# Kernel tuning notes

Measured on AMD Instinct MI355X. Metric: run time of the kernel, lower is better.

Reference implementation:

```python
import jax, jax.numpy as jnp
import numpy as np

NOISE_STD = 0.5
NOISE_VAR = NOISE_STD ** 2  # softmax temperature = 1 / noise_variance

N, C, H, W = 256, 3, 32, 32
M = 50000


def setup_inputs() -> dict:
    key = jax.random.key(0)
    k1, k2 = jax.random.split(key)
    x = jax.random.normal(k1, (N, C, H, W), dtype=jnp.float32)
    dataset = jax.random.normal(k2, (M, C, H, W), dtype=jnp.float32)
    return {"x": x, "dataset": dataset}


def reference(x, dataset):
    # Flatten: x -> [N, D], dataset -> [M, D]
    n = x.shape[0]
    input_shape = dataset.shape[1:]
    xf = x.reshape(n, -1)
    df = dataset.reshape(dataset.shape[0], -1)
    # scores = x . dataset^T / noise_variance, softmax over dataset axis
    scores = jnp.einsum("nd,md->nm", xf, df) / NOISE_VAR  # [N, M]
    w = jax.nn.softmax(scores, axis=-1)
    # Weighted average of dataset points: [N, D]
    out = jnp.einsum("nm,md->nd", w, df)
    return out.reshape((n,) + input_shape)
```

## Files before the change

### kernel.cpp

```cpp
#include <hip/hip_runtime.h>
#include <stdint.h>
#include <stddef.h>

#define N_Q 256
#define M_D 50000
#define K_D 3072
#define MTILE 64
#define BK 32
#define CAND_CAP 128
#define WINDOW 9.0f

typedef short bf16x8 __attribute__((ext_vector_type(8)));
typedef float f32x4 __attribute__((ext_vector_type(4)));

static __device__ inline unsigned short f2bf(float f) {
    unsigned int u = __float_as_uint(f);
    u += 0x7fffu + ((u >> 16) & 1u);
    return (unsigned short)(u >> 16);
}

__global__ __launch_bounds__(256) void cvt_x_kernel(const float* __restrict__ x,
                                                    short* __restrict__ xb) {
    int i = (blockIdx.x * 256 + threadIdx.x) * 4;
    float4 f = *(const float4*)(x + i);
    ushort4 o;
    o.x = f2bf(f.x); o.y = f2bf(f.y); o.z = f2bf(f.z); o.w = f2bf(f.w);
    *(ushort4*)(xb + i) = o;
}

__global__ __launch_bounds__(256) void gemm_scores(const short* __restrict__ xb,
                                                   const float* __restrict__ dset,
                                                   float* __restrict__ scores) {
    __shared__ __align__(16) short sA[N_Q * BK];
    __shared__ __align__(16) short sB[MTILE * BK];

    const int tid = threadIdx.x;
    const int w = tid >> 6;
    const int l = tid & 63;
    const int m0 = blockIdx.x * MTILE;

    f32x4 acc[4][4];
#pragma unroll
    for (int i = 0; i < 4; ++i)
#pragma unroll
        for (int j = 0; j < 4; ++j)
            acc[i][j] = (f32x4){0.f, 0.f, 0.f, 0.f};

    const int br = tid >> 2;
    const int bq = tid & 3;
    const bool bvalid = (m0 + br) < M_D;
    const float* bsrc = dset + (size_t)(m0 + br) * K_D + bq * 8;

    const int kk = (l >> 4) * 8;
    const int rA = l & 15;

    for (int kt = 0; kt < K_D / BK; ++kt) {
        __syncthreads();

#pragma unroll
        for (int j = 0; j < 4; ++j) {
            int c = j * 256 + tid;
            int row = c >> 2;
            int off = c & 3;
            bf16x8 v = *(const bf16x8*)(xb + (size_t)row * K_D + kt * BK + off * 8);
            *(bf16x8*)&sA[c * 8] = v;
        }
        {
            bf16x8 pk;
            if (bvalid) {
                const float* p = bsrc + kt * BK;
                float4 f0 = *(const float4*)p;
                float4 f1 = *(const float4*)(p + 4);
                pk[0] = (short)f2bf(f0.x); pk[1] = (short)f2bf(f0.y);
                pk[2] = (short)f2bf(f0.z); pk[3] = (short)f2bf(f0.w);
                pk[4] = (short)f2bf(f1.x); pk[5] = (short)f2bf(f1.y);
                pk[6] = (short)f2bf(f1.z); pk[7] = (short)f2bf(f1.w);
            } else {
                pk = (bf16x8){0, 0, 0, 0, 0, 0, 0, 0};
            }
            *(bf16x8*)&sB[br * BK + bq * 8] = pk;
        }
        __syncthreads();

        bf16x8 af[4], bfr[4];
#pragma unroll
        for (int ai = 0; ai < 4; ++ai)
            af[ai] = *(const bf16x8*)&sA[(w * 64 + ai * 16 + rA) * BK + kk];
#pragma unroll
        for (int bj = 0; bj < 4; ++bj)
            bfr[bj] = *(const bf16x8*)&sB[(bj * 16 + rA) * BK + kk];
#pragma unroll
        for (int ai = 0; ai < 4; ++ai)
#pragma unroll
            for (int bj = 0; bj < 4; ++bj)
                acc[ai][bj] = __builtin_amdgcn_mfma_f32_16x16x32_bf16(
                    af[ai], bfr[bj], acc[ai][bj], 0, 0, 0);
    }

    const int crow = (l >> 4) * 4;
    const int ccol = l & 15;
#pragma unroll
    for (int ai = 0; ai < 4; ++ai) {
#pragma unroll
        for (int bj = 0; bj < 4; ++bj) {
            int m = m0 + bj * 16 + ccol;
            if (m < M_D) {
#pragma unroll
                for (int r = 0; r < 4; ++r) {
                    int n = w * 64 + ai * 16 + crow + r;
                    scores[(size_t)n * M_D + m] = acc[ai][bj][r];
                }
            }
        }
    }
}

__global__ __launch_bounds__(256) void scan_rows(const float* __restrict__ scores,
                                                 int* __restrict__ cidx,
                                                 int* __restrict__ ccnt) {
    const int n = blockIdx.x;
    const int tid = threadIdx.x;
    const float4* row4 = (const float4*)(scores + (size_t)n * M_D);

    float mx = -3.0e38f;
    for (int m4 = tid; m4 < M_D / 4; m4 += 256) {
        float4 v = row4[m4];
        mx = fmaxf(mx, fmaxf(fmaxf(v.x, v.y), fmaxf(v.z, v.w)));
    }
#pragma unroll
    for (int off = 32; off > 0; off >>= 1) mx = fmaxf(mx, __shfl_down(mx, off));

    __shared__ float wred[4];
    __shared__ int cnt;
    if ((tid & 63) == 0) wred[tid >> 6] = mx;
    if (tid == 0) cnt = 0;
    __syncthreads();
    float rowmax = fmaxf(fmaxf(wred[0], wred[1]), fmaxf(wred[2], wred[3]));
    float thr = rowmax - WINDOW;

    for (int m4 = tid; m4 < M_D / 4; m4 += 256) {
        float4 v = row4[m4];
        if (v.x >= thr || v.y >= thr || v.z >= thr || v.w >= thr) {
            float e[4] = {v.x, v.y, v.z, v.w};
#pragma unroll
            for (int j = 0; j < 4; ++j) {
                if (e[j] >= thr) {
                    int p = atomicAdd(&cnt, 1);
                    if (p < CAND_CAP) cidx[n * CAND_CAP + p] = m4 * 4 + j;
                }
            }
        }
    }
    __syncthreads();
    if (tid == 0) ccnt[n] = cnt < CAND_CAP ? cnt : CAND_CAP;
}

__global__ __launch_bounds__(256) void finalize_rows(const float* __restrict__ x,
                                                     const float* __restrict__ dset,
                                                     const int* __restrict__ cidx,
                                                     const int* __restrict__ ccnt,
                                                     float* __restrict__ out) {
    const int n = blockIdx.x;
    const int tid = threadIdx.x;
    const int cnt = ccnt[n];

    __shared__ float L[CAND_CAP];
    __shared__ float wred[4];
    const float4* xr4 = (const float4*)(x + (size_t)n * K_D);

    for (int c = 0; c < cnt; ++c) {
        const float4* dr4 = (const float4*)(dset + (size_t)cidx[n * CAND_CAP + c] * K_D);
        float p = 0.f;
        for (int j = tid; j < K_D / 4; j += 256) {
            float4 a = xr4[j], b = dr4[j];
            p += a.x * b.x + a.y * b.y + a.z * b.z + a.w * b.w;
        }
#pragma unroll
        for (int off = 32; off > 0; off >>= 1) p += __shfl_down(p, off);
        if ((tid & 63) == 0) wred[tid >> 6] = p;
        __syncthreads();
        if (tid == 0) L[c] = 4.0f * (wred[0] + wred[1] + wred[2] + wred[3]);
        __syncthreads();
    }

    if (tid == 0) {
        float mx = -3.0e38f;
        for (int c = 0; c < cnt; ++c) mx = fmaxf(mx, L[c]);
        float s = 0.f;
        for (int c = 0; c < cnt; ++c) { float e = expf(L[c] - mx); L[c] = e; s += e; }
        float inv = 1.0f / s;
        for (int c = 0; c < cnt; ++c) L[c] *= inv;
    }
    __syncthreads();

    float4* out4 = (float4*)(out + (size_t)n * K_D);
    for (int j = tid; j < K_D / 4; j += 256) {
        float4 o = {0.f, 0.f, 0.f, 0.f};
        for (int c = 0; c < cnt; ++c) {
            float wc = L[c];
            float4 d = *(const float4*)(dset + (size_t)cidx[n * CAND_CAP + c] * K_D + j * 4);
            o.x += wc * d.x; o.y += wc * d.y; o.z += wc * d.z; o.w += wc * d.w;
        }
        out4[j] = o;
    }
}

extern "C" void kernel_launch(void* const* d_in, const int* in_sizes, int n_in,
                              void* d_out, int out_size, void* d_ws, size_t ws_size,
                              hipStream_t stream) {
    const float* x = (const float*)d_in[0];
    const float* dset = (const float*)d_in[1];
    float* out = (float*)d_out;

    char* ws = (char*)d_ws;
    short* xb = (short*)ws;
    float* scores = (float*)(ws + 1572864);
    int* cidx = (int*)(ws + 1572864 + 51200000);
    int* ccnt = (int*)(ws + 1572864 + 51200000 + 131072);

    cvt_x_kernel<<<768, 256, 0, stream>>>(x, xb);
    gemm_scores<<<(M_D + MTILE - 1) / MTILE, 256, 0, stream>>>(xb, dset, scores);
    scan_rows<<<N_Q, 256, 0, stream>>>(scores, cidx, ccnt);
    finalize_rows<<<N_Q, 256, 0, stream>>>(x, dset, cidx, ccnt, out);
}
```

Before: 962.7 us.

## Restructure GEMM loads with direct-to-LDS, swizzle, prefetch; split row scan

The score GEMM now uses BK=64 with XOR-swizzled LDS layouts to reduce bank conflicts. The bf16 query tile is loaded straight into LDS via global_load_lds, and the next dataset K-slice is prefetched into registers during the MFMA work. The per-row scan is split into a rowmax kernel and a collect kernel, each using 8 blocks per row with global atomics, to raise parallelism. The finalize dot products now give each wave its own candidate, which removes per-candidate block barriers. The larger LDS footprint may reduce occupancy, and the extra kernel launch adds overhead.

New measurement: 912.5 us. 5.2% less time.

```diff
diff --git a/kernel.cpp b/kernel.cpp
--- a/kernel.cpp
+++ b/kernel.cpp
@@ -5,18 +5,26 @@
 #define N_Q 256
 #define M_D 50000
 #define K_D 3072
-#define MTILE 64
-#define BK 32
+#define MT 64
+#define BK 64
+#define NKT (K_D / BK)
 #define CAND_CAP 128
 #define WINDOW 9.0f
+#define SPLIT 8
 
 typedef short bf16x8 __attribute__((ext_vector_type(8)));
 typedef float f32x4 __attribute__((ext_vector_type(4)));
 
-static __device__ inline unsigned short f2bf(float f) {
+static __device__ __forceinline__ unsigned short f2bf(float f) {
     unsigned int u = __float_as_uint(f);
     u += 0x7fffu + ((u >> 16) & 1u);
     return (unsigned short)(u >> 16);
+}
+
+static __device__ __forceinline__ void load_lds16(const short* g, short* l) {
+    __builtin_amdgcn_global_load_lds(
+        (const __attribute__((address_space(1))) void*)g,
+        (__attribute__((address_space(3))) void*)l, 16, 0, 0);
 }
 
 __global__ __launch_bounds__(256) void cvt_x_kernel(const float* __restrict__ x,
@@ -32,12 +40,12 @@
                                                    const float* __restrict__ dset,
                                                    float* __restrict__ scores) {
     __shared__ __align__(16) short sA[N_Q * BK];
-    __shared__ __align__(16) short sB[MTILE * BK];
+    __shared__ __align__(16) short sB[MT * BK];
 
     const int tid = threadIdx.x;
     const int w = tid >> 6;
     const int l = tid & 63;
-    const int m0 = blockIdx.x * MTILE;
+    const int m0 = blockIdx.x * MT;
 
     f32x4 acc[4][4];
 #pragma unroll
@@ -46,55 +54,74 @@
         for (int j = 0; j < 4; ++j)
             acc[i][j] = (f32x4){0.f, 0.f, 0.f, 0.f};
 
-    const int br = tid >> 2;
-    const int bq = tid & 3;
-    const bool bvalid = (m0 + br) < M_D;
-    const float* bsrc = dset + (size_t)(m0 + br) * K_D + bq * 8;
-
-    const int kk = (l >> 4) * 8;
+    const int ar = l >> 3;
+    const int aq = (l & 7) ^ ar;
+    const short* abase = xb + (size_t)(w * 8 + ar) * K_D + aq * 8;
+    short* adst = &sA[w * 512];
+
+    const int r1 = tid >> 3;
+    const int q1 = tid & 7;
+    const int r2 = r1 + 32;
+    const bool v1 = (m0 + r1) < M_D;
+    const bool v2 = (m0 + r2) < M_D;
+    const float* b1 = dset + (size_t)(m0 + r1) * K_D + q1 * 8;
+    const float* b2 = dset + (size_t)(m0 + r2) * K_D + q1 * 8;
+    short* w1p = &sB[(size_t)((r1 << 3) + (q1 ^ (r1 & 7))) << 3];
+    short* w2p = &sB[(size_t)((r2 << 3) + (q1 ^ (r2 & 7))) << 3];
+
+    float4 f0a = {0,0,0,0}, f0b = {0,0,0,0}, f1a = {0,0,0,0}, f1b = {0,0,0,0};
+    if (v1) { f0a = *(const float4*)b1; f0b = *(const float4*)(b1 + 4); }
+    if (v2) { f1a = *(const float4*)b2; f1b = *(const float4*)(b2 + 4); }
+
     const int rA = l & 15;
-
-    for (int kt = 0; kt < K_D / BK; ++kt) {
+    const int r7 = l & 7;
+    const int kq = l >> 4;
+
+    for (int kt = 0; kt < NKT; ++kt) {
         __syncthreads();
 
 #pragma unroll
-        for (int j = 0; j < 4; ++j) {
-            int c = j * 256 + tid;
-            int row = c >> 2;
-            int off = c & 3;
-            bf16x8 v = *(const bf16x8*)(xb + (size_t)row * K_D + kt * BK + off * 8);
-            *(bf16x8*)&sA[c * 8] = v;
-        }
+        for (int j = 0; j < 8; ++j)
+            load_lds16(abase + (size_t)j * (32 * K_D) + kt * BK, adst + j * 2048);
+
         {
-            bf16x8 pk;
-            if (bvalid) {
-                const float* p = bsrc + kt * BK;
-                float4 f0 = *(const float4*)p;
-                float4 f1 = *(const float4*)(p + 4);
-                pk[0] = (short)f2bf(f0.x); pk[1] = (short)f2bf(f0.y);
-                pk[2] = (short)f2bf(f0.z); pk[3] = (short)f2bf(f0.w);
-                pk[4] = (short)f2bf(f1.x); pk[5] = (short)f2bf(f1.y);
-                pk[6] = (short)f2bf(f1.z); pk[7] = (short)f2bf(f1.w);
-            } else {
-                pk = (bf16x8){0, 0, 0, 0, 0, 0, 0, 0};
-            }
-            *(bf16x8*)&sB[br * BK + bq * 8] = pk;
+            bf16x8 p;
+            p[0] = (short)f2bf(f0a.x); p[1] = (short)f2bf(f0a.y);
+            p[2] = (short)f2bf(f0a.z); p[3] = (short)f2bf(f0a.w);
+            p[4] = (short)f2bf(f0b.x); p[5] = (short)f2bf(f0b.y);
+            p[6] = (short)f2bf(f0b.z); p[7] = (short)f2bf(f0b.w);
+            *(bf16x8*)w1p = p;
+            p[0] = (short)f2bf(f1a.x); p[1] = (short)f2bf(f1a.y);
+            p[2] = (short)f2bf(f1a.z); p[3] = (short)f2bf(f1a.w);
+            p[4] = (short)f2bf(f1b.x); p[5] = (short)f2bf(f1b.y);
+            p[6] = (short)f2bf(f1b.z); p[7] = (short)f2bf(f1b.w);
+            *(bf16x8*)w2p = p;
         }
         __syncthreads();
 
-        bf16x8 af[4], bfr[4];
-#pragma unroll
-        for (int ai = 0; ai < 4; ++ai)
-            af[ai] = *(const bf16x8*)&sA[(w * 64 + ai * 16 + rA) * BK + kk];
-#pragma unroll
-        for (int bj = 0; bj < 4; ++bj)
-            bfr[bj] = *(const bf16x8*)&sB[(bj * 16 + rA) * BK + kk];
-#pragma unroll
-        for (int ai = 0; ai < 4; ++ai)
+        if (kt + 1 < NKT) {
+            const int o = (kt + 1) * BK;
+            if (v1) { f0a = *(const float4*)(b1 + o); f0b = *(const float4*)(b1 + o + 4); }
+            if (v2) { f1a = *(const float4*)(b2 + o); f1b = *(const float4*)(b2 + o + 4); }
+        }
+
+#pragma unroll
+        for (int h = 0; h < 2; ++h) {
+            const int qs = (((h * 4 + kq) ^ r7) << 3);
+            bf16x8 af[4], bfr[4];
+#pragma unroll
+            for (int ai = 0; ai < 4; ++ai)
+                af[ai] = *(const bf16x8*)&sA[(size_t)(w * 64 + ai * 16 + rA) * 64 + qs];
 #pragma unroll
             for (int bj = 0; bj < 4; ++bj)
-                acc[ai][bj] = __builtin_amdgcn_mfma_f32_16x16x32_bf16(
-                    af[ai], bfr[bj], acc[ai][bj], 0, 0, 0);
+                bfr[bj] = *(const bf16x8*)&sB[(size_t)(bj * 16 + rA) * 64 + qs];
+#pragma unroll
+            for (int ai = 0; ai < 4; ++ai)
+#pragma unroll
+                for (int bj = 0; bj < 4; ++bj)
+                    acc[ai][bj] = __builtin_amdgcn_mfma_f32_16x16x32_bf16(
+                        af[ai], bfr[bj], acc[ai][bj], 0, 0, 0);
+        }
     }
 
     const int crow = (l >> 4) * 4;
@@ -115,44 +142,63 @@
     }
 }
 
-__global__ __launch_bounds__(256) void scan_rows(const float* __restrict__ scores,
-                                                 int* __restrict__ cidx,
-                                                 int* __restrict__ ccnt) {
-    const int n = blockIdx.x;
+__global__ __launch_bounds__(256) void rowmax_kernel(const float* __restrict__ scores,
+                                                     float* __restrict__ pmax,
+                                                     int* __restrict__ ccnt) {
+    const int n = blockIdx.x >> 3;
+    const int s = blockIdx.x & 7;
     const int tid = threadIdx.x;
     const float4* row4 = (const float4*)(scores + (size_t)n * M_D);
+    const int start = s * 1563;
+    int end = start + 1563; if (end > M_D / 4) end = M_D / 4;
 
     float mx = -3.0e38f;
-    for (int m4 = tid; m4 < M_D / 4; m4 += 256) {
-        float4 v = row4[m4];
+    for (int i = start + tid; i < end; i += 256) {
+        float4 v = row4[i];
         mx = fmaxf(mx, fmaxf(fmaxf(v.x, v.y), fmaxf(v.z, v.w)));
     }
 #pragma unroll
     for (int off = 32; off > 0; off >>= 1) mx = fmaxf(mx, __shfl_down(mx, off));
 
     __shared__ float wred[4];
-    __shared__ int cnt;
     if ((tid & 63) == 0) wred[tid >> 6] = mx;
-    if (tid == 0) cnt = 0;
     __syncthreads();
-    float rowmax = fmaxf(fmaxf(wred[0], wred[1]), fmaxf(wred[2], wred[3]));
-    float thr = rowmax - WINDOW;
-
-    for (int m4 = tid; m4 < M_D / 4; m4 += 256) {
-        float4 v = row4[m4];
+    if (tid == 0) {
+        pmax[blockIdx.x] = fmaxf(fmaxf(wred[0], wred[1]), fmaxf(wred[2], wred[3]));
+        if (s == 0) ccnt[n] = 0;
+    }
+}
+
+__global__ __launch_bounds__(256) void collect_kernel(const float* __restrict__ scores,
+                                                      const float* __restrict__ pmax,
+                                                      int* __restrict__ cidx,
+                                                      int* __restrict__ ccnt) {
+    const int n = blockIdx.x >> 3;
+    const int s = blockIdx.x & 7;
+    const int tid = threadIdx.x;
+
+    float rm = -3.0e38f;
+#pragma unroll
+    for (int i = 0; i < 8; ++i) rm = fmaxf(rm, pmax[n * 8 + i]);
+    const float thr = rm - WINDOW;
+
+    const float4* row4 = (const float4*)(scores + (size_t)n * M_D);
+    const int start = s * 1563;
+    int end = start + 1563; if (end > M_D / 4) end = M_D / 4;
+
+    for (int i = start + tid; i < end; i += 256) {
+        float4 v = row4[i];
         if (v.x >= thr || v.y >= thr || v.z >= thr || v.w >= thr) {
             float e[4] = {v.x, v.y, v.z, v.w};
 #pragma unroll
             for (int j = 0; j < 4; ++j) {
                 if (e[j] >= thr) {
-                    int p = atomicAdd(&cnt, 1);
-                    if (p < CAND_CAP) cidx[n * CAND_CAP + p] = m4 * 4 + j;
+                    int p = atomicAdd(&ccnt[n], 1);
+                    if (p < CAND_CAP) cidx[n * CAND_CAP + p] = i * 4 + j;
                 }
             }
         }
     }
-    __syncthreads();
-    if (tid == 0) ccnt[n] = cnt < CAND_CAP ? cnt : CAND_CAP;
 }
 
 __global__ __launch_bounds__(256) void finalize_rows(const float* __restrict__ x,
@@ -162,26 +208,24 @@
                                                      float* __restrict__ out) {
     const int n = blockIdx.x;
     const int tid = threadIdx.x;
-    const int cnt = ccnt[n];
+    const int w = tid >> 6, l = tid & 63;
+    int cnt = ccnt[n]; if (cnt > CAND_CAP) cnt = CAND_CAP;
 
     __shared__ float L[CAND_CAP];
-    __shared__ float wred[4];
     const float4* xr4 = (const float4*)(x + (size_t)n * K_D);
 
-    for (int c = 0; c < cnt; ++c) {
+    for (int c = w; c < cnt; c += 4) {
         const float4* dr4 = (const float4*)(dset + (size_t)cidx[n * CAND_CAP + c] * K_D);
         float p = 0.f;
-        for (int j = tid; j < K_D / 4; j += 256) {
+        for (int j = l; j < K_D / 4; j += 64) {
             float4 a = xr4[j], b = dr4[j];
             p += a.x * b.x + a.y * b.y + a.z * b.z + a.w * b.w;
         }
 #pragma unroll
         for (int off = 32; off > 0; off >>= 1) p += __shfl_down(p, off);
-        if ((tid & 63) == 0) wred[tid >> 6] = p;
-        __syncthreads();
-        if (tid == 0) L[c] = 4.0f * (wred[0] + wred[1] + wred[2] + wred[3]);
-        __syncthreads();
-    }
+        if (l == 0) L[c] = 4.0f * p;
+    }
+    __syncthreads();
 
     if (tid == 0) {
         float mx = -3.0e38f;
@@ -215,11 +259,13 @@
     char* ws = (char*)d_ws;
     short* xb = (short*)ws;
     float* scores = (float*)(ws + 1572864);
-    int* cidx = (int*)(ws + 1572864 + 51200000);
-    int* ccnt = (int*)(ws + 1572864 + 51200000 + 131072);
+    float* pmax   = (float*)(ws + 1572864 + 51200000);
+    int* cidx     = (int*)(ws + 1572864 + 51200000 + 8192);
+    int* ccnt     = (int*)(ws + 1572864 + 51200000 + 8192 + 131072);
 
     cvt_x_kernel<<<768, 256, 0, stream>>>(x, xb);
-    gemm_scores<<<(M_D + MTILE - 1) / MTILE, 256, 0, stream>>>(xb, dset, scores);
-    scan_rows<<<N_Q, 256, 0, stream>>>(scores, cidx, ccnt);
+    gemm_scores<<<(M_D + MT - 1) / MT, 256, 0, stream>>>(xb, dset, scores);
+    rowmax_kernel<<<N_Q * SPLIT, 256, 0, stream>>>(scores, pmax, ccnt);
+    collect_kernel<<<N_Q * SPLIT, 256, 0, stream>>>(scores, pmax, cidx, ccnt);
     finalize_rows<<<N_Q, 256, 0, stream>>>(x, dset, cidx, ccnt, out);
 }
```
